# Kernel optimization log

Hardware: AMD Instinct MI355X
Metric: run time of the kernel (lower is better)

## Reference

```python
import jax, jax.numpy as jnp
import numpy as np

ALPHA = 1.0
EPS = 1e-9
MASK_FILL = 100000.0  # large value pushes masked entries to the end of ascending sort


def setup_inputs() -> dict:
    key = jax.random.key(0)
    k1, k2, k3, k4 = jax.random.split(key, 4)
    bs, nh, n = 128, 32, 2048
    input1 = jax.random.normal(k1, (bs, 4, nh, n), dtype=jnp.float32)
    input2 = jax.random.normal(k2, (bs, 1, nh, n), dtype=jnp.float32)
    mask1 = jax.random.randint(k3, (bs, 4, nh, n), 0, 2).astype(jnp.int32)
    mask2 = jax.random.randint(k4, (bs, 1, nh, n), 0, 2).astype(jnp.int32)
    return {"input1": input1, "mask1": mask1, "input2": input2, "mask2": mask2}


def reference(input1, mask1, input2, mask2):
    # input1: (bs, 4, nh, n) scores; input2/mask2: (bs, 1, nh, n) targets/mask.
    # mask1 is unused by the original forward.
    i2 = jnp.where(mask2 > 0, input2, jnp.float32(MASK_FILL))
    idx = jnp.argsort(i2, axis=-1)                                  # (bs, 1, nh, n)
    mask_sorted = jnp.take_along_axis(mask2, idx, axis=-1).astype(jnp.float32)
    idx4 = jnp.broadcast_to(idx, input1.shape)                      # repeat over the 4 choices
    inputs_sorted = jnp.take_along_axis(input1, idx4, axis=-1)      # (bs, 4, nh, n)
    proj = jnp.exp(ALPHA * inputs_sorted) * mask_sorted             # mode='exp'
    proj_cum = jnp.cumsum(proj, axis=-1) * mask_sorted
    prob = jnp.prod((proj + EPS) / (proj_cum + EPS), axis=-1)       # (bs, 4, nh)
    return jnp.transpose(prob, (0, 2, 1))                           # (bs, nh, 4)
```

## Files before the change

kernel.cpp:

```cpp
#include <hip/hip_runtime.h>

#define N   2048
#define NT  256
#define EPK 32

typedef unsigned int u32;

__device__ __forceinline__ u32 fkey(float f) {
  u32 u = __float_as_uint(f);
  return (u & 0x80000000u) ? ~u : (u | 0x80000000u);
}

__device__ __forceinline__ u32 umin32(u32 a, u32 b) { return a < b ? a : b; }
__device__ __forceinline__ u32 umax32(u32 a, u32 b) { return a < b ? b : a; }

template <int D>
__device__ __forceinline__ u32 exch(u32 x, int lane) {
  if constexpr (D == 1) {
    return (u32)__builtin_amdgcn_update_dpp((int)x, (int)x, 0xB1, 0xF, 0xF, true);
  } else if constexpr (D == 2) {
    return (u32)__builtin_amdgcn_update_dpp((int)x, (int)x, 0x4E, 0xF, 0xF, true);
  } else if constexpr (D == 4) {
    return (u32)__builtin_amdgcn_ds_swizzle((int)x, 0x101F);
  } else if constexpr (D == 8) {
    return (u32)__builtin_amdgcn_update_dpp((int)x, (int)x, 0x128, 0xF, 0xF, true);
  } else if constexpr (D == 16) {
    return (u32)__builtin_amdgcn_ds_swizzle((int)x, 0x401F);
  } else {
    int a = (int)x, b = (int)x;
    asm("v_permlane32_swap_b32 %0, %1" : "+v"(a), "+v"(b));
    return (lane & 32) ? (u32)a : (u32)b;
  }
}

template <int D>
__device__ __forceinline__ void sh_pass(u32* kv, bool keep_min, int lane) {
#pragma unroll
  for (int m = 0; m < EPK; ++m) {
    u32 o = exch<D>(kv[m], lane);
    u32 mn = umin32(kv[m], o), mx = umax32(kv[m], o);
    kv[m] = keep_min ? mn : mx;
  }
}

#define INPASS(J, UPEXPR)                               \
  {                                                     \
    _Pragma("unroll")                                   \
    for (int m = 0; m < EPK; ++m)                       \
      if ((m & (J)) == 0) {                             \
        const bool up_ = (UPEXPR);                      \
        u32 x = kv[m], y = kv[m | (J)];                 \
        u32 mn = umin32(x, y), mx = umax32(x, y);       \
        kv[m] = up_ ? mn : mx;                          \
        kv[m | (J)] = up_ ? mx : mn;                    \
      }                                                 \
  }

__global__ __launch_bounds__(NT, 4) void listmle_kernel(
    const float* __restrict__ input1,
    const float* __restrict__ input2,
    const int* __restrict__ mask2,
    float* __restrict__ out) {
  __shared__ __align__(16) float rows[4][N];

  const int tid = threadIdx.x;
  const int lane = tid & 63;
  const int wv = tid >> 6;
  const int p = blockIdx.x * 4 + wv;
  const int lane32 = lane * EPK;

  u32* keys = (u32*)rows[wv];
  {
    const float4* i2v = (const float4*)(input2 + (size_t)p * N);
    const int4* m2v = (const int4*)(mask2 + (size_t)p * N);
#pragma unroll
    for (int q = 0; q < 8; ++q) {
      float4 vv = i2v[lane + 64 * q];
      int4 mm = m2v[lane + 64 * q];
      const u32 i0 = (u32)(4 * (lane + 64 * q));
      float vs[4] = {vv.x, vv.y, vv.z, vv.w};
      int ms[4] = {mm.x, mm.y, mm.z, mm.w};
#pragma unroll
      for (int r = 0; r < 4; ++r) {
        u32 idx = i0 + r;
        u32 key = (ms[r] > 0) ? ((fkey(vs[r]) & 0xFFFFF800u) | idx)
                              : (0xFFFFF800u | idx);
        keys[idx ^ ((idx >> 5) & 31u)] = key;
      }
    }
  }
  u32 kv[EPK];
#pragma unroll
  for (int m = 0; m < EPK; ++m) {
    u32 idx = (u32)(lane32 + m);
    kv[m] = keys[idx ^ ((u32)lane & 31u)];
  }

  INPASS(1, (m & 2) == 0)
  INPASS(2, (m & 4) == 0) INPASS(1, (m & 4) == 0)
  INPASS(4, (m & 8) == 0) INPASS(2, (m & 8) == 0) INPASS(1, (m & 8) == 0)
  INPASS(8, (m & 16) == 0) INPASS(4, (m & 16) == 0)
  INPASS(2, (m & 16) == 0) INPASS(1, (m & 16) == 0)
  {
    const bool up = (lane & 1) == 0;
    INPASS(16, up) INPASS(8, up) INPASS(4, up) INPASS(2, up) INPASS(1, up)
  }
  {
    const bool up = (lane & 2) == 0;
    sh_pass<1>(kv, ((lane & 1) == 0) == up, lane);
    INPASS(16, up) INPASS(8, up) INPASS(4, up) INPASS(2, up) INPASS(1, up)
  }
  {
    const bool up = (lane & 4) == 0;
    sh_pass<2>(kv, ((lane & 2) == 0) == up, lane);
    sh_pass<1>(kv, ((lane & 1) == 0) == up, lane);
    INPASS(16, up) INPASS(8, up) INPASS(4, up) INPASS(2, up) INPASS(1, up)
  }
  {
    const bool up = (lane & 8) == 0;
    sh_pass<4>(kv, ((lane & 4) == 0) == up, lane);
    sh_pass<2>(kv, ((lane & 2) == 0) == up, lane);
    sh_pass<1>(kv, ((lane & 1) == 0) == up, lane);
    INPASS(16, up) INPASS(8, up) INPASS(4, up) INPASS(2, up) INPASS(1, up)
  }
  {
    const bool up = (lane & 16) == 0;
    sh_pass<8>(kv, ((lane & 8) == 0) == up, lane);
    sh_pass<4>(kv, ((lane & 4) == 0) == up, lane);
    sh_pass<2>(kv, ((lane & 2) == 0) == up, lane);
    sh_pass<1>(kv, ((lane & 1) == 0) == up, lane);
    INPASS(16, up) INPASS(8, up) INPASS(4, up) INPASS(2, up) INPASS(1, up)
  }
  {
    const bool up = (lane & 32) == 0;
    sh_pass<16>(kv, ((lane & 16) == 0) == up, lane);
    sh_pass<8>(kv, ((lane & 8) == 0) == up, lane);
    sh_pass<4>(kv, ((lane & 4) == 0) == up, lane);
    sh_pass<2>(kv, ((lane & 2) == 0) == up, lane);
    sh_pass<1>(kv, ((lane & 1) == 0) == up, lane);
    INPASS(16, up) INPASS(8, up) INPASS(4, up) INPASS(2, up) INPASS(1, up)
  }
  {
    sh_pass<32>(kv, (lane & 32) == 0, lane);
    sh_pass<16>(kv, (lane & 16) == 0, lane);
    sh_pass<8>(kv, (lane & 8) == 0, lane);
    sh_pass<4>(kv, (lane & 4) == 0, lane);
    sh_pass<2>(kv, (lane & 2) == 0, lane);
    sh_pass<1>(kv, (lane & 1) == 0, lane);
    INPASS(16, true) INPASS(8, true) INPASS(4, true) INPASS(2, true)
    INPASS(1, true)
  }

  u32 pk[EPK / 2];
#pragma unroll
  for (int t = 0; t < EPK / 2; ++t) {
    u32 a = kv[2 * t], b = kv[2 * t + 1];
    u32 ia = (a & 0x7FFu) | ((a < 0xFFFFF800u) ? 0x800u : 0u);
    u32 ib = (b & 0x7FFu) | ((b < 0xFFFFF800u) ? 0x800u : 0u);
    pk[t] = ia | (ib << 16);
  }

  const int b = p >> 5, h = p & 31;
  float* rowbuf = rows[wv];
  for (int c = 0; c < 4; ++c) {
    const float* r1 = input1 + ((size_t)((b * 4 + c) * 32 + h)) * N;
#pragma unroll
    for (int q = 0; q < 8; ++q)
      ((float4*)rowbuf)[lane + 64 * q] = ((const float4*)r1)[lane + 64 * q];

    float e[EPK];
    float lsum = 0.f;
#pragma unroll
    for (int m = 0; m < EPK; ++m) {
      u32 info = (pk[m >> 1] >> ((m & 1) * 16)) & 0xFFFFu;
      float v = rowbuf[info & 0x7FFu];
      float pe = (info & 0x800u) ? __expf(v) : 0.f;
      e[m] = pe;
      lsum += pe;
    }

    float inc = lsum;
#pragma unroll
    for (int d = 1; d < 64; d <<= 1) {
      float o = __shfl_up(inc, d, 64);
      if (lane >= d) inc += o;
    }
    float cum = inc - lsum;

    float prod = 1.f;
#pragma unroll
    for (int m = 0; m < EPK; ++m) {
      cum += e[m];
      u32 info = pk[m >> 1] >> ((m & 1) * 16);
      if (info & 0x800u) prod *= __fdividef(e[m] + 1e-9f, cum + 1e-9f);
    }
#pragma unroll
    for (int d = 1; d < 64; d <<= 1) prod *= __shfl_xor(prod, d, 64);
    if (lane == 0) out[(size_t)p * 4 + c] = prod;
  }
}

extern "C" void kernel_launch(void* const* d_in, const int* in_sizes, int n_in,
                              void* d_out, int out_size, void* d_ws, size_t ws_size,
                              hipStream_t stream) {
  const float* input1 = (const float*)d_in[0];
  const float* input2 = (const float*)d_in[2];
  const int* mask2 = (const int*)d_in[3];
  float* out = (float*)d_out;

  const int problems = 128 * 32;
  listmle_kernel<<<problems / 4, NT, 0, stream>>>(input1, input2, mask2, out);
}
```

Baseline: 72.68 us.

## Split each sort row across two wavefronts and prefetch input1 rows into registers

```diff
diff --git a/kernel.cpp b/kernel.cpp
--- a/kernel.cpp
+++ b/kernel.cpp
@@ -1,8 +1,8 @@
 #include <hip/hip_runtime.h>
 
 #define N   2048
-#define NT  256
-#define EPK 32
+#define NT  128
+#define EPK 16
 
 typedef unsigned int u32;
 
@@ -56,28 +56,29 @@
       }                                                 \
   }
 
-__global__ __launch_bounds__(NT, 4) void listmle_kernel(
+__global__ __launch_bounds__(NT, 8) void listmle_kernel(
     const float* __restrict__ input1,
     const float* __restrict__ input2,
     const int* __restrict__ mask2,
     float* __restrict__ out) {
-  __shared__ __align__(16) float rows[4][N];
+  __shared__ __align__(16) float rows[N];
+  __shared__ float hand[2];
 
   const int tid = threadIdx.x;
   const int lane = tid & 63;
-  const int wv = tid >> 6;
-  const int p = blockIdx.x * 4 + wv;
-  const int lane32 = lane * EPK;
-
-  u32* keys = (u32*)rows[wv];
+  const int w = tid >> 6;
+  const int p = blockIdx.x;
+  const int b = p >> 5, h = p & 31;
+
+  u32* keys = (u32*)rows;
   {
     const float4* i2v = (const float4*)(input2 + (size_t)p * N);
     const int4* m2v = (const int4*)(mask2 + (size_t)p * N);
 #pragma unroll
-    for (int q = 0; q < 8; ++q) {
-      float4 vv = i2v[lane + 64 * q];
-      int4 mm = m2v[lane + 64 * q];
-      const u32 i0 = (u32)(4 * (lane + 64 * q));
+    for (int q = 0; q < 4; ++q) {
+      float4 vv = i2v[tid + 128 * q];
+      int4 mm = m2v[tid + 128 * q];
+      const u32 i0 = 4u * (u32)(tid + 128 * q);
       float vs[4] = {vv.x, vv.y, vv.z, vv.w};
       int ms[4] = {mm.x, mm.y, mm.z, mm.w};
 #pragma unroll
@@ -89,39 +90,47 @@
       }
     }
   }
+
+  float4 pf[4];
+  {
+    const float4* r1 = (const float4*)(input1 + ((size_t)((b * 4 + 0) * 32 + h)) * N);
+#pragma unroll
+    for (int q = 0; q < 4; ++q) pf[q] = r1[tid + 128 * q];
+  }
+
+  __syncthreads();
   u32 kv[EPK];
 #pragma unroll
   for (int m = 0; m < EPK; ++m) {
-    u32 idx = (u32)(lane32 + m);
-    kv[m] = keys[idx ^ ((u32)lane & 31u)];
-  }
+    u32 idx = (u32)(w * 1024 + lane * EPK + m);
+    kv[m] = keys[idx ^ ((idx >> 5) & 31u)];
+  }
+  __syncthreads();
 
   INPASS(1, (m & 2) == 0)
   INPASS(2, (m & 4) == 0) INPASS(1, (m & 4) == 0)
   INPASS(4, (m & 8) == 0) INPASS(2, (m & 8) == 0) INPASS(1, (m & 8) == 0)
-  INPASS(8, (m & 16) == 0) INPASS(4, (m & 16) == 0)
-  INPASS(2, (m & 16) == 0) INPASS(1, (m & 16) == 0)
   {
     const bool up = (lane & 1) == 0;
-    INPASS(16, up) INPASS(8, up) INPASS(4, up) INPASS(2, up) INPASS(1, up)
+    INPASS(8, up) INPASS(4, up) INPASS(2, up) INPASS(1, up)
   }
   {
     const bool up = (lane & 2) == 0;
     sh_pass<1>(kv, ((lane & 1) == 0) == up, lane);
-    INPASS(16, up) INPASS(8, up) INPASS(4, up) INPASS(2, up) INPASS(1, up)
+    INPASS(8, up) INPASS(4, up) INPASS(2, up) INPASS(1, up)
   }
   {
     const bool up = (lane & 4) == 0;
     sh_pass<2>(kv, ((lane & 2) == 0) == up, lane);
     sh_pass<1>(kv, ((lane & 1) == 0) == up, lane);
-    INPASS(16, up) INPASS(8, up) INPASS(4, up) INPASS(2, up) INPASS(1, up)
+    INPASS(8, up) INPASS(4, up) INPASS(2, up) INPASS(1, up)
   }
   {
     const bool up = (lane & 8) == 0;
     sh_pass<4>(kv, ((lane & 4) == 0) == up, lane);
     sh_pass<2>(kv, ((lane & 2) == 0) == up, lane);
     sh_pass<1>(kv, ((lane & 1) == 0) == up, lane);
-    INPASS(16, up) INPASS(8, up) INPASS(4, up) INPASS(2, up) INPASS(1, up)
+    INPASS(8, up) INPASS(4, up) INPASS(2, up) INPASS(1, up)
   }
   {
     const bool up = (lane & 16) == 0;
@@ -129,7 +138,7 @@
     sh_pass<4>(kv, ((lane & 4) == 0) == up, lane);
     sh_pass<2>(kv, ((lane & 2) == 0) == up, lane);
     sh_pass<1>(kv, ((lane & 1) == 0) == up, lane);
-    INPASS(16, up) INPASS(8, up) INPASS(4, up) INPASS(2, up) INPASS(1, up)
+    INPASS(8, up) INPASS(4, up) INPASS(2, up) INPASS(1, up)
   }
   {
     const bool up = (lane & 32) == 0;
@@ -138,42 +147,64 @@
     sh_pass<4>(kv, ((lane & 4) == 0) == up, lane);
     sh_pass<2>(kv, ((lane & 2) == 0) == up, lane);
     sh_pass<1>(kv, ((lane & 1) == 0) == up, lane);
-    INPASS(16, up) INPASS(8, up) INPASS(4, up) INPASS(2, up) INPASS(1, up)
-  }
-  {
+    INPASS(8, up) INPASS(4, up) INPASS(2, up) INPASS(1, up)
+  }
+  {
+    const bool up = (w == 0);
+    sh_pass<32>(kv, ((lane & 32) == 0) == up, lane);
+    sh_pass<16>(kv, ((lane & 16) == 0) == up, lane);
+    sh_pass<8>(kv, ((lane & 8) == 0) == up, lane);
+    sh_pass<4>(kv, ((lane & 4) == 0) == up, lane);
+    sh_pass<2>(kv, ((lane & 2) == 0) == up, lane);
+    sh_pass<1>(kv, ((lane & 1) == 0) == up, lane);
+    INPASS(8, up) INPASS(4, up) INPASS(2, up) INPASS(1, up)
+  }
+  {
+    u32* ex = (u32*)rows;
+#pragma unroll
+    for (int m = 0; m < EPK; ++m) ex[w * 1024 + m * 64 + lane] = kv[m];
+    __syncthreads();
+#pragma unroll
+    for (int m = 0; m < EPK; ++m) {
+      u32 o = ex[(w ^ 1) * 1024 + m * 64 + lane];
+      kv[m] = (w == 0) ? umin32(kv[m], o) : umax32(kv[m], o);
+    }
+    __syncthreads();
     sh_pass<32>(kv, (lane & 32) == 0, lane);
     sh_pass<16>(kv, (lane & 16) == 0, lane);
     sh_pass<8>(kv, (lane & 8) == 0, lane);
     sh_pass<4>(kv, (lane & 4) == 0, lane);
     sh_pass<2>(kv, (lane & 2) == 0, lane);
     sh_pass<1>(kv, (lane & 1) == 0, lane);
-    INPASS(16, true) INPASS(8, true) INPASS(4, true) INPASS(2, true)
-    INPASS(1, true)
+    INPASS(8, true) INPASS(4, true) INPASS(2, true) INPASS(1, true)
   }
 
   u32 pk[EPK / 2];
 #pragma unroll
   for (int t = 0; t < EPK / 2; ++t) {
-    u32 a = kv[2 * t], b = kv[2 * t + 1];
+    u32 a = kv[2 * t], b2 = kv[2 * t + 1];
     u32 ia = (a & 0x7FFu) | ((a < 0xFFFFF800u) ? 0x800u : 0u);
-    u32 ib = (b & 0x7FFu) | ((b < 0xFFFFF800u) ? 0x800u : 0u);
+    u32 ib = (b2 & 0x7FFu) | ((b2 < 0xFFFFF800u) ? 0x800u : 0u);
     pk[t] = ia | (ib << 16);
   }
 
-  const int b = p >> 5, h = p & 31;
-  float* rowbuf = rows[wv];
   for (int c = 0; c < 4; ++c) {
-    const float* r1 = input1 + ((size_t)((b * 4 + c) * 32 + h)) * N;
-#pragma unroll
-    for (int q = 0; q < 8; ++q)
-      ((float4*)rowbuf)[lane + 64 * q] = ((const float4*)r1)[lane + 64 * q];
+#pragma unroll
+    for (int q = 0; q < 4; ++q) ((float4*)rows)[tid + 128 * q] = pf[q];
+    __syncthreads();
+    if (c < 3) {
+      const float4* r1 =
+          (const float4*)(input1 + ((size_t)((b * 4 + c + 1) * 32 + h)) * N);
+#pragma unroll
+      for (int q = 0; q < 4; ++q) pf[q] = r1[tid + 128 * q];
+    }
 
     float e[EPK];
     float lsum = 0.f;
 #pragma unroll
     for (int m = 0; m < EPK; ++m) {
       u32 info = (pk[m >> 1] >> ((m & 1) * 16)) & 0xFFFFu;
-      float v = rowbuf[info & 0x7FFu];
+      float v = rows[info & 0x7FFu];
       float pe = (info & 0x800u) ? __expf(v) : 0.f;
       e[m] = pe;
       lsum += pe;
@@ -185,18 +216,36 @@
       float o = __shfl_up(inc, d, 64);
       if (lane >= d) inc += o;
     }
-    float cum = inc - lsum;
-
-    float prod = 1.f;
-#pragma unroll
-    for (int m = 0; m < EPK; ++m) {
-      cum += e[m];
-      u32 info = pk[m >> 1] >> ((m & 1) * 16);
-      if (info & 0x800u) prod *= __fdividef(e[m] + 1e-9f, cum + 1e-9f);
-    }
-#pragma unroll
-    for (int d = 1; d < 64; d <<= 1) prod *= __shfl_xor(prod, d, 64);
-    if (lane == 0) out[(size_t)p * 4 + c] = prod;
+    float excl = inc - lsum;
+
+    if (w == 0) {
+      float cum = excl;
+      float prod = 1.f;
+#pragma unroll
+      for (int m = 0; m < EPK; ++m) {
+        cum += e[m];
+        u32 info = pk[m >> 1] >> ((m & 1) * 16);
+        if (info & 0x800u) prod *= __fdividef(e[m] + 1e-9f, cum + 1e-9f);
+      }
+#pragma unroll
+      for (int d = 1; d < 64; d <<= 1) prod *= __shfl_xor(prod, d, 64);
+      if (lane == 63) hand[0] = inc;
+      if (lane == 0) hand[1] = prod;
+    }
+    __syncthreads();
+    if (w == 1) {
+      float cum = hand[0] + excl;
+      float prod = 1.f;
+#pragma unroll
+      for (int m = 0; m < EPK; ++m) {
+        cum += e[m];
+        u32 info = pk[m >> 1] >> ((m & 1) * 16);
+        if (info & 0x800u) prod *= __fdividef(e[m] + 1e-9f, cum + 1e-9f);
+      }
+#pragma unroll
+      for (int d = 1; d < 64; d <<= 1) prod *= __shfl_xor(prod, d, 64);
+      if (lane == 0) out[(size_t)p * 4 + c] = hand[1] * prod;
+    }
   }
 }
 
@@ -209,5 +258,5 @@
   float* out = (float*)d_out;
 
   const int problems = 128 * 32;
-  listmle_kernel<<<problems / 4, NT, 0, stream>>>(input1, input2, mask2, out);
-}
+  listmle_kernel<<<problems, NT, 0, stream>>>(input1, input2, mask2, out);
+}
```

After: 84.19 us. +15.8%, slower.
